# Kernel optimization log

Hardware: AMD Instinct MI355X
Metric: run time of the kernel (lower is better)

The kernel has to match this reference:

```python
import jax, jax.numpy as jnp
import numpy as np

DIM = 1024
NUM_HEADS = 16
HEAD_DIM = DIM // NUM_HEADS
SCALE = HEAD_DIM ** -0.5


def setup_inputs() -> dict:
    key = jax.random.key(0)
    k1, k2, k3, k4, k5 = jax.random.split(key, 5)
    B, N, C = 2, 2048, DIM
    x = jax.random.normal(k1, (B, N, C), dtype=jnp.float32)
    # nn.Linear(dim, 3*dim, bias=False): weight shape [3*dim, dim]
    w_qkv = jax.random.normal(k2, (3 * C, C), dtype=jnp.float32) * (C ** -0.5)
    # nn.Linear(dim, dim): weight [dim, dim], bias [dim]
    w_proj = jax.random.normal(k3, (C, C), dtype=jnp.float32) * (C ** -0.5)
    b_proj = jax.random.normal(k4, (C,), dtype=jnp.float32) * 0.02
    return {"x": x, "w_qkv": w_qkv, "w_proj": w_proj, "b_proj": b_proj}


def reference(x, w_qkv, w_proj, b_proj):
    B, N, C = x.shape
    H, D = NUM_HEADS, HEAD_DIM
    # qkv: [B, N, 3C] -> [3, B, H, N, D]
    qkv = (x @ w_qkv.T).reshape(B, N, 3, H, D).transpose(2, 0, 3, 1, 4)
    q, k, v = qkv[0], qkv[1], qkv[2]
    # attention scores [B, H, N, N]
    attn = jnp.einsum("bhnd,bhmd->bhnm", q, k) * SCALE
    attn = jax.nn.softmax(attn, axis=-1)
    # dropout p=0.0 -> identity (eval mode)
    out = jnp.einsum("bhnm,bhmd->bhnd", attn, v)  # [B, H, N, D]
    out = out.transpose(0, 2, 1, 3).reshape(B, N, C)
    return out @ w_proj.T + b_proj
```

## Files before the change

### kernel.cpp

```cpp
#include <hip/hip_runtime.h>
#include <hip/hip_bf16.h>
#include <cstdint>

#define DEV __device__ __forceinline__

typedef float f32x4 __attribute__((ext_vector_type(4)));
typedef short bf16x8 __attribute__((ext_vector_type(8)));
typedef unsigned short u16;
typedef unsigned int u32;

constexpr int Bb = 2, Nn = 2048, Cc = 1024, Hh = 16, Dd = 64;
constexpr float QSCALE = 0.18033688011112042f;

DEV u16 f2b(float f) {
  unsigned u = __float_as_uint(f);
  u += 0x7FFFu + ((u >> 16) & 1u);
  return (u16)(u >> 16);
}

DEV void gload_lds16(const u16* g, u16* l) {
  __builtin_amdgcn_global_load_lds(
      (const __attribute__((address_space(1))) void*)g,
      (__attribute__((address_space(3))) void*)l, 16, 0, 0);
}

DEV int swz(int row, int byteInRow) {
  return row * 128 + (byteInRow ^ ((row & 7) << 4));
}
DEV int swzp(int row, int byteInRow) {
  return row * 64 + (byteInRow ^ ((((row >> 2) + row) & 3) << 4));
}

DEV u32 cvtpk(float lo, float hi) {
  u32 r;
  asm("v_cvt_pk_bf16_f32 %0, %1, %2" : "=v"(r) : "v"(lo), "v"(hi));
  return r;
}
DEV void pl32swap(u32& a, u32& b) {
  asm("v_permlane32_swap_b32 %0, %1" : "+v"(a), "+v"(b));
}
DEV void pl16swap(u32& a, u32& b) {
  asm("v_permlane16_swap_b32 %0, %1" : "+v"(a), "+v"(b));
}

#if __has_builtin(__builtin_amdgcn_exp2f)
DEV float fast_exp2(float x) { return __builtin_amdgcn_exp2f(x); }
#else
DEV float fast_exp2(float x) { return exp2f(x); }
#endif

__global__ void cvt_all(const float* __restrict__ x, u16* __restrict__ xb,
                        const float* __restrict__ wq, u16* __restrict__ wqb,
                        const float* __restrict__ wp, u16* __restrict__ wpb) {
  constexpr int n1 = 4096 * 1024 / 4, n2 = 3072 * 1024 / 4, n3 = 1024 * 1024 / 4;
  constexpr int nQ = 1024 * 1024 / 4;
  int idx = blockIdx.x * blockDim.x + threadIdx.x;
  int stride = gridDim.x * blockDim.x;
  for (int i = idx; i < n1 + n2 + n3; i += stride) {
    const float* in; u16* out; int j;
    float sc = 1.f;
    if (i < n1) { in = x; out = xb; j = i; }
    else if (i < n1 + n2) { in = wq; out = wqb; j = i - n1; if (j < nQ) sc = QSCALE; }
    else { in = wp; out = wpb; j = i - n1 - n2; }
    float4 v = ((const float4*)in)[j];
    ushort4 o;
    o.x = f2b(v.x * sc); o.y = f2b(v.y * sc); o.z = f2b(v.z * sc); o.w = f2b(v.w * sc);
    ((ushort4*)out)[j] = o;
  }
}

__global__ __launch_bounds__(256) void gemm_qkv(
    const u16* __restrict__ A, const u16* __restrict__ W, u16* __restrict__ qkv_out) {
  constexpr int K = 1024, NT = K / 32;
  __shared__ __align__(16) u16 As[2][128 * 32];
  __shared__ __align__(16) u16 Bs[2][128 * 32];
  const int t = threadIdx.x, lane = t & 63;
  const int wm = t >> 7, wn = (t >> 6) & 1;
  const int bid = blockIdx.x;
  const int wg = (bid & 7) * 96 + (bid >> 3);
  const int bx = wg % 24, by = wg / 24;
  const int m0 = by * 128, n0 = bx * 128;
  const int fr = lane & 15, g = lane >> 4;

  const int srow = t >> 2;
  const int scp = (t & 3) ^ (((t >> 2) + (t >> 4)) & 3);
  const u16* gA = A + (size_t)(m0 + srow) * K + scp * 8;
  const u16* gW = W + (size_t)(n0 + srow) * K + scp * 8;

  f32x4 acc[4][4] = {};

#define STAGEQ(tile, buf)                                              \
  {                                                                    \
    const int k0_ = (tile) * 32;                                       \
    gload_lds16(gA + k0_, &As[buf][t * 8]);                            \
    gload_lds16(gA + k0_ + (size_t)64 * K, &As[buf][t * 8 + 2048]);    \
    gload_lds16(gW + k0_, &Bs[buf][t * 8]);                            \
    gload_lds16(gW + k0_ + (size_t)64 * K, &Bs[buf][t * 8 + 2048]);    \
  }

  STAGEQ(0, 0);
  __syncthreads();

  for (int tt = 0; tt < NT; ++tt) {
    const int cur = tt & 1;
    if (tt + 1 < NT) STAGEQ(tt + 1, cur ^ 1);
    const char* Ac = (const char*)As[cur];
    const char* Bc = (const char*)Bs[cur];
    bf16x8 af[4], bfr[4];
#pragma unroll
    for (int i = 0; i < 4; ++i)
      af[i] = *(const bf16x8*)(Ac + swzp(wm * 64 + i * 16 + fr, g * 16));
#pragma unroll
    for (int j = 0; j < 4; ++j)
      bfr[j] = *(const bf16x8*)(Bc + swzp(wn * 64 + j * 16 + fr, g * 16));
    __builtin_amdgcn_s_setprio(1);
#pragma unroll
    for (int i = 0; i < 4; ++i)
#pragma unroll
      for (int j = 0; j < 4; ++j)
        acc[i][j] = __builtin_amdgcn_mfma_f32_16x16x32_bf16(af[i], bfr[j], acc[i][j], 0, 0, 0);
    __builtin_amdgcn_s_setprio(0);
    __syncthreads();
  }

  const int rg = g * 4;
#pragma unroll
  for (int mi = 0; mi < 4; ++mi) {
#pragma unroll
    for (int ni = 0; ni < 4; ++ni) {
      const int col = n0 + wn * 64 + ni * 16 + fr;
      const int s = col >> 10, h = (col >> 6) & 15, d = col & 63;
      const int row0 = m0 + wm * 64 + mi * 16 + rg;
      const int b = row0 >> 11, nb = row0 & 2047;
      if (s == 2) {
        ushort4 o4;
        o4.x = f2b(acc[mi][ni][0]); o4.y = f2b(acc[mi][ni][1]);
        o4.z = f2b(acc[mi][ni][2]); o4.w = f2b(acc[mi][ni][3]);
        const size_t off = (size_t)2 * Bb * Hh * Nn * Dd +
                           (((size_t)b * Hh + h) * Dd + d) * Nn + nb;
        *(ushort4*)&qkv_out[off] = o4;
      } else {
#pragma unroll
        for (int r = 0; r < 4; ++r) {
          const size_t off = ((((size_t)s * Bb + b) * Hh + h) * Nn + (nb + r)) * Dd + d;
          qkv_out[off] = f2b(acc[mi][ni][r]);
        }
      }
    }
  }
#undef STAGEQ
}

__global__ __launch_bounds__(256) void gemm_proj(
    const u16* __restrict__ A, const u16* __restrict__ W,
    float* __restrict__ fout, const float* __restrict__ bias) {
  constexpr int K = 1024, Nmat = 1024, NT = K / 32;
  __shared__ __align__(16) u16 As[2][128 * 32];
  __shared__ __align__(16) u16 Bs[2][128 * 32];
  const int t = threadIdx.x, lane = t & 63;
  const int wm = t >> 7, wn = (t >> 6) & 1;
  const int bid = blockIdx.x;
  const int wg = (bid & 7) * 32 + (bid >> 3);
  const int bx = wg & 7, by = wg >> 3;
  const int m0 = by * 128, n0 = bx * 128;
  const int fr = lane & 15, g = lane >> 4;

  const int srow = t >> 2;
  const int scp = (t & 3) ^ (((t >> 2) + (t >> 4)) & 3);
  const u16* gA = A + (size_t)(m0 + srow) * K + scp * 8;
  const u16* gW = W + (size_t)(n0 + srow) * K + scp * 8;

  f32x4 acc[4][4] = {};

#define STAGEP(tile, buf)                                              \
  {                                                                    \
    const int k0_ = (tile) * 32;                                       \
    gload_lds16(gA + k0_, &As[buf][t * 8]);                            \
    gload_lds16(gA + k0_ + (size_t)64 * K, &As[buf][t * 8 + 2048]);    \
    gload_lds16(gW + k0_, &Bs[buf][t * 8]);                            \
    gload_lds16(gW + k0_ + (size_t)64 * K, &Bs[buf][t * 8 + 2048]);    \
  }

  STAGEP(0, 0);
  __syncthreads();

  for (int tt = 0; tt < NT; ++tt) {
    const int cur = tt & 1;
    if (tt + 1 < NT) STAGEP(tt + 1, cur ^ 1);
    const char* Ac = (const char*)As[cur];
    const char* Bc = (const char*)Bs[cur];
    bf16x8 af[4], bfr[4];
#pragma unroll
    for (int i = 0; i < 4; ++i)
      af[i] = *(const bf16x8*)(Ac + swzp(wm * 64 + i * 16 + fr, g * 16));
#pragma unroll
    for (int j = 0; j < 4; ++j)
      bfr[j] = *(const bf16x8*)(Bc + swzp(wn * 64 + j * 16 + fr, g * 16));
    __builtin_amdgcn_s_setprio(1);
#pragma unroll
    for (int i = 0; i < 4; ++i)
#pragma unroll
      for (int j = 0; j < 4; ++j)
        acc[i][j] = __builtin_amdgcn_mfma_f32_16x16x32_bf16(af[i], bfr[j], acc[i][j], 0, 0, 0);
    __builtin_amdgcn_s_setprio(0);
    __syncthreads();
  }

  const int rg = g * 4;
#pragma unroll
  for (int i = 0; i < 4; ++i)
#pragma unroll
    for (int j = 0; j < 4; ++j) {
      const int col = n0 + wn * 64 + j * 16 + fr;
#pragma unroll
      for (int r = 0; r < 4; ++r) {
        const int row = m0 + wm * 64 + i * 16 + rg + r;
        fout[(size_t)row * Nmat + col] = acc[i][j][r] + bias[col];
      }
    }
#undef STAGEP
}

__global__ __launch_bounds__(512, 4) void attn_fwd(
    const u16* __restrict__ Qg, const u16* __restrict__ Kg,
    const u16* __restrict__ Vtg, u16* __restrict__ Og) {
  __shared__ __align__(16) char smem[34816];
  const int t = threadIdx.x, lane = t & 63, w = t >> 6;
  const int qg = w >> 1, kh = w & 1;
  const int wg = ((blockIdx.x & 7) << 6) | (blockIdx.x >> 3);
  const int bh = wg >> 4;
  const int q0 = (wg & 15) * 128;
  const size_t base = (size_t)bh * Nn * Dd;
  const u16* Qb = Qg + base;
  const u16* Kb = Kg + base;
  const u16* Vb = Vtg + base;
  const int fr = lane & 15, g = lane >> 4;

  bf16x8 onesv;
  {
    union { u32 u[4]; bf16x8 v; } o_;
#pragma unroll
    for (int i = 0; i < 4; ++i) o_.u[i] = 0x3F803F80u;
    onesv = o_.v;
  }

  bf16x8 qf[2][2];
#pragma unroll
  for (int qt = 0; qt < 2; ++qt)
#pragma unroll
    for (int dc = 0; dc < 2; ++dc)
      qf[qt][dc] = *(const bf16x8*)&Qb[(size_t)(q0 + qg * 32 + qt * 16 + fr) * 64 + dc * 32 + g * 8];

  f32x4 ot[4][2] = {};
  float lse[2] = {0.f, 0.f};

  const int srow = t >> 3, scb = t & 7;
  const u16* kp = Kb + srow * 64 + scb * 8;
  const u16* vp = Vb + (size_t)srow * Nn + scb * 8;
  uint4 kreg, vreg;

#define LOADT(tile)                                        \
  {                                                        \
    kreg = *(const uint4*)(kp + (size_t)(tile) * 4096);    \
    vreg = *(const uint4*)(vp + (size_t)(tile) * 64);      \
  }
#define STORET(buf)                                        \
  {                                                        \
    char* kb_ = smem + (buf) * 16384;                      \
    *(uint4*)(kb_ + swz(srow, scb * 16)) = kreg;           \
    *(uint4*)(kb_ + 8192 + swz(srow, scb * 16)) = vreg;    \
  }

  LOADT(0);
  STORET(0);
  __syncthreads();

  for (int it = 0; it < 32; ++it) {
    const int cur = it & 1;
    const char* Kst = smem + cur * 16384;
    const char* Vst = Kst + 8192;
    if (it < 31) LOADT(it + 1);

    bf16x8 kf[2][2];
#pragma unroll
    for (int kvt = 0; kvt < 2; ++kvt)
#pragma unroll
      for (int dc = 0; dc < 2; ++dc)
        kf[kvt][dc] = *(const bf16x8*)(Kst + swz(kh * 32 + kvt * 16 + fr, dc * 64 + g * 16));
    f32x4 st[2][2] = {};
    __builtin_amdgcn_s_setprio(1);
#pragma unroll
    for (int dc = 0; dc < 2; ++dc)
#pragma unroll
      for (int kvt = 0; kvt < 2; ++kvt)
#pragma unroll
        for (int qt = 0; qt < 2; ++qt)
          st[kvt][qt] = __builtin_amdgcn_mfma_f32_16x16x32_bf16(kf[kvt][dc], qf[qt][dc], st[kvt][qt], 0, 0, 0);
    __builtin_amdgcn_s_setprio(0);

#pragma unroll
    for (int kvt = 0; kvt < 2; ++kvt)
#pragma unroll
      for (int qt = 0; qt < 2; ++qt)
#pragma unroll
        for (int r = 0; r < 4; ++r)
          st[kvt][qt][r] = fast_exp2(st[kvt][qt][r]);

    u32 pw[2][4];
#pragma unroll
    for (int qt = 0; qt < 2; ++qt) {
      u32 a0 = cvtpk(st[0][qt][0], st[0][qt][1]);
      u32 a1 = cvtpk(st[0][qt][2], st[0][qt][3]);
      u32 b0 = cvtpk(st[1][qt][0], st[1][qt][1]);
      u32 b1 = cvtpk(st[1][qt][2], st[1][qt][3]);
      pl32swap(a0, b0); pl16swap(a0, b0);
      pl32swap(a1, b1); pl16swap(a1, b1);
      pw[qt][0] = a0; pw[qt][1] = a1; pw[qt][2] = b0; pw[qt][3] = b1;
    }

    bf16x8 vf[4];
#pragma unroll
    for (int dt = 0; dt < 4; ++dt)
      vf[dt] = *(const bf16x8*)(Vst + swz(dt * 16 + fr, kh * 64 + g * 16));
    __builtin_amdgcn_s_setprio(1);
#pragma unroll
    for (int qt = 0; qt < 2; ++qt) {
      union { u32 u[4]; bf16x8 v; } pu;
      pu.u[0] = pw[qt][0]; pu.u[1] = pw[qt][1]; pu.u[2] = pw[qt][2]; pu.u[3] = pw[qt][3];
      f32x4 z = {0.f, 0.f, 0.f, 0.f};
      f32x4 rsv = __builtin_amdgcn_mfma_f32_16x16x32_bf16(onesv, pu.v, z, 0, 0, 0);
      lse[qt] += rsv[0];
#pragma unroll
      for (int dt = 0; dt < 4; ++dt)
        ot[dt][qt] = __builtin_amdgcn_mfma_f32_16x16x32_bf16(vf[dt], pu.v, ot[dt][qt], 0, 0, 0);
    }
    __builtin_amdgcn_s_setprio(0);

    if (it < 31) {
      STORET(cur ^ 1);
      __syncthreads();
    }
  }

  __syncthreads();
  float* Ob = (float*)(smem + qg * 8448);
  float* Lb = (float*)(smem + 33792 + qg * 128);
  if (kh) {
#pragma unroll
    for (int qt = 0; qt < 2; ++qt) {
#pragma unroll
      for (int dt = 0; dt < 4; ++dt)
#pragma unroll
        for (int r = 0; r < 4; ++r)
          Ob[(qt * 16 + fr) * 66 + dt * 16 + 4 * g + r] = ot[dt][qt][r];
      if (g == 0) Lb[qt * 16 + fr] = lse[qt];
    }
  }
  __syncthreads();
  if (!kh) {
    const int b = bh >> 4, h = bh & 15;
#pragma unroll
    for (int qt = 0; qt < 2; ++qt) {
      const float inv = 1.f / (lse[qt] + Lb[qt * 16 + fr]);
      const int tok = q0 + qg * 32 + qt * 16 + fr;
      const size_t rowbase = ((size_t)b * Nn + tok) * Cc + h * 64;
#pragma unroll
      for (int dt = 0; dt < 4; ++dt) {
        ushort4 o4;
        o4.x = f2b((ot[dt][qt][0] + Ob[(qt * 16 + fr) * 66 + dt * 16 + 4 * g + 0]) * inv);
        o4.y = f2b((ot[dt][qt][1] + Ob[(qt * 16 + fr) * 66 + dt * 16 + 4 * g + 1]) * inv);
        o4.z = f2b((ot[dt][qt][2] + Ob[(qt * 16 + fr) * 66 + dt * 16 + 4 * g + 2]) * inv);
        o4.w = f2b((ot[dt][qt][3] + Ob[(qt * 16 + fr) * 66 + dt * 16 + 4 * g + 3]) * inv);
        *(ushort4*)&Og[rowbase + dt * 16 + g * 4] = o4;
      }
    }
  }
#undef LOADT
#undef STORET
}

extern "C" void kernel_launch(void* const* d_in, const int* in_sizes, int n_in,
                              void* d_out, int out_size, void* d_ws, size_t ws_size,
                              hipStream_t stream) {
  const float* x      = (const float*)d_in[0];
  const float* w_qkv  = (const float*)d_in[1];
  const float* w_proj = (const float*)d_in[2];
  const float* b_proj = (const float*)d_in[3];
  float* out = (float*)d_out;

  u16* xb     = (u16*)d_ws;
  u16* wqkvb  = xb + (size_t)4096 * 1024;
  u16* wprojb = wqkvb + (size_t)3072 * 1024;
  u16* qkv    = wprojb + (size_t)1024 * 1024;
  u16* ows    = qkv + (size_t)3 * Bb * Hh * Nn * Dd;
  u16* q  = qkv;
  u16* k  = qkv + (size_t)Bb * Hh * Nn * Dd;
  u16* vt = k + (size_t)Bb * Hh * Nn * Dd;

  cvt_all<<<2048, 256, 0, stream>>>(x, xb, w_qkv, wqkvb, w_proj, wprojb);
  gemm_qkv<<<768, 256, 0, stream>>>(xb, wqkvb, qkv);
  attn_fwd<<<512, 512, 0, stream>>>(q, k, vt, ows);
  gemm_proj<<<256, 256, 0, stream>>>(ows, wprojb, out, b_proj);
}
```

Before: 114.4 us.

## Halve attention query tile per block to double grid size and occupancy

Result: slower. 158.1 us (+38.2%).

```diff
diff --git a/kernel.cpp b/kernel.cpp
--- a/kernel.cpp
+++ b/kernel.cpp
@@ -221,15 +221,15 @@
 #undef STAGEP
 }
 
-__global__ __launch_bounds__(512, 4) void attn_fwd(
+__global__ __launch_bounds__(512, 8) void attn_fwd(
     const u16* __restrict__ Qg, const u16* __restrict__ Kg,
     const u16* __restrict__ Vtg, u16* __restrict__ Og) {
   __shared__ __align__(16) char smem[34816];
   const int t = threadIdx.x, lane = t & 63, w = t >> 6;
   const int qg = w >> 1, kh = w & 1;
-  const int wg = ((blockIdx.x & 7) << 6) | (blockIdx.x >> 3);
-  const int bh = wg >> 4;
-  const int q0 = (wg & 15) * 128;
+  const int wg = ((blockIdx.x & 7) << 7) | (blockIdx.x >> 3);
+  const int bh = wg >> 5;
+  const int q0 = (wg & 31) * 64;
   const size_t base = (size_t)bh * Nn * Dd;
   const u16* Qb = Qg + base;
   const u16* Kb = Kg + base;
@@ -244,15 +244,13 @@
     onesv = o_.v;
   }
 
-  bf16x8 qf[2][2];
-#pragma unroll
-  for (int qt = 0; qt < 2; ++qt)
-#pragma unroll
-    for (int dc = 0; dc < 2; ++dc)
-      qf[qt][dc] = *(const bf16x8*)&Qb[(size_t)(q0 + qg * 32 + qt * 16 + fr) * 64 + dc * 32 + g * 8];
-
-  f32x4 ot[4][2] = {};
-  float lse[2] = {0.f, 0.f};
+  bf16x8 qf[2];
+#pragma unroll
+  for (int dc = 0; dc < 2; ++dc)
+    qf[dc] = *(const bf16x8*)&Qb[(size_t)(q0 + qg * 16 + fr) * 64 + dc * 32 + g * 8];
+
+  f32x4 ot[4] = {};
+  float lse = 0.f;
 
   const int srow = t >> 3, scb = t & 7;
   const u16* kp = Kb + srow * 64 + scb * 8;
@@ -287,52 +285,42 @@
 #pragma unroll
       for (int dc = 0; dc < 2; ++dc)
         kf[kvt][dc] = *(const bf16x8*)(Kst + swz(kh * 32 + kvt * 16 + fr, dc * 64 + g * 16));
-    f32x4 st[2][2] = {};
+    f32x4 st[2] = {};
     __builtin_amdgcn_s_setprio(1);
 #pragma unroll
     for (int dc = 0; dc < 2; ++dc)
 #pragma unroll
       for (int kvt = 0; kvt < 2; ++kvt)
-#pragma unroll
-        for (int qt = 0; qt < 2; ++qt)
-          st[kvt][qt] = __builtin_amdgcn_mfma_f32_16x16x32_bf16(kf[kvt][dc], qf[qt][dc], st[kvt][qt], 0, 0, 0);
+        st[kvt] = __builtin_amdgcn_mfma_f32_16x16x32_bf16(kf[kvt][dc], qf[dc], st[kvt], 0, 0, 0);
     __builtin_amdgcn_s_setprio(0);
 
 #pragma unroll
     for (int kvt = 0; kvt < 2; ++kvt)
 #pragma unroll
-      for (int qt = 0; qt < 2; ++qt)
-#pragma unroll
-        for (int r = 0; r < 4; ++r)
-          st[kvt][qt][r] = fast_exp2(st[kvt][qt][r]);
-
-    u32 pw[2][4];
-#pragma unroll
-    for (int qt = 0; qt < 2; ++qt) {
-      u32 a0 = cvtpk(st[0][qt][0], st[0][qt][1]);
-      u32 a1 = cvtpk(st[0][qt][2], st[0][qt][3]);
-      u32 b0 = cvtpk(st[1][qt][0], st[1][qt][1]);
-      u32 b1 = cvtpk(st[1][qt][2], st[1][qt][3]);
-      pl32swap(a0, b0); pl16swap(a0, b0);
-      pl32swap(a1, b1); pl16swap(a1, b1);
-      pw[qt][0] = a0; pw[qt][1] = a1; pw[qt][2] = b0; pw[qt][3] = b1;
-    }
+      for (int r = 0; r < 4; ++r)
+        st[kvt][r] = fast_exp2(st[kvt][r]);
+
+    u32 a0 = cvtpk(st[0][0], st[0][1]);
+    u32 a1 = cvtpk(st[0][2], st[0][3]);
+    u32 b0 = cvtpk(st[1][0], st[1][1]);
+    u32 b1 = cvtpk(st[1][2], st[1][3]);
+    pl32swap(a0, b0); pl16swap(a0, b0);
+    pl32swap(a1, b1); pl16swap(a1, b1);
 
     bf16x8 vf[4];
 #pragma unroll
     for (int dt = 0; dt < 4; ++dt)
       vf[dt] = *(const bf16x8*)(Vst + swz(dt * 16 + fr, kh * 64 + g * 16));
     __builtin_amdgcn_s_setprio(1);
-#pragma unroll
-    for (int qt = 0; qt < 2; ++qt) {
+    {
       union { u32 u[4]; bf16x8 v; } pu;
-      pu.u[0] = pw[qt][0]; pu.u[1] = pw[qt][1]; pu.u[2] = pw[qt][2]; pu.u[3] = pw[qt][3];
+      pu.u[0] = a0; pu.u[1] = a1; pu.u[2] = b0; pu.u[3] = b1;
       f32x4 z = {0.f, 0.f, 0.f, 0.f};
       f32x4 rsv = __builtin_amdgcn_mfma_f32_16x16x32_bf16(onesv, pu.v, z, 0, 0, 0);
-      lse[qt] += rsv[0];
+      lse += rsv[0];
 #pragma unroll
       for (int dt = 0; dt < 4; ++dt)
-        ot[dt][qt] = __builtin_amdgcn_mfma_f32_16x16x32_bf16(vf[dt], pu.v, ot[dt][qt], 0, 0, 0);
+        ot[dt] = __builtin_amdgcn_mfma_f32_16x16x32_bf16(vf[dt], pu.v, ot[dt], 0, 0, 0);
     }
     __builtin_amdgcn_s_setprio(0);
 
@@ -343,36 +331,30 @@
   }
 
   __syncthreads();
-  float* Ob = (float*)(smem + qg * 8448);
-  float* Lb = (float*)(smem + 33792 + qg * 128);
+  float* Ob = (float*)(smem + qg * 4224);
+  float* Lb = (float*)(smem + 16896 + qg * 64);
   if (kh) {
 #pragma unroll
-    for (int qt = 0; qt < 2; ++qt) {
-#pragma unroll
-      for (int dt = 0; dt < 4; ++dt)
-#pragma unroll
-        for (int r = 0; r < 4; ++r)
-          Ob[(qt * 16 + fr) * 66 + dt * 16 + 4 * g + r] = ot[dt][qt][r];
-      if (g == 0) Lb[qt * 16 + fr] = lse[qt];
-    }
+    for (int dt = 0; dt < 4; ++dt)
+#pragma unroll
+      for (int r = 0; r < 4; ++r)
+        Ob[fr * 66 + dt * 16 + 4 * g + r] = ot[dt][r];
+    if (g == 0) Lb[fr] = lse;
   }
   __syncthreads();
   if (!kh) {
     const int b = bh >> 4, h = bh & 15;
-#pragma unroll
-    for (int qt = 0; qt < 2; ++qt) {
-      const float inv = 1.f / (lse[qt] + Lb[qt * 16 + fr]);
-      const int tok = q0 + qg * 32 + qt * 16 + fr;
-      const size_t rowbase = ((size_t)b * Nn + tok) * Cc + h * 64;
-#pragma unroll
-      for (int dt = 0; dt < 4; ++dt) {
-        ushort4 o4;
-        o4.x = f2b((ot[dt][qt][0] + Ob[(qt * 16 + fr) * 66 + dt * 16 + 4 * g + 0]) * inv);
-        o4.y = f2b((ot[dt][qt][1] + Ob[(qt * 16 + fr) * 66 + dt * 16 + 4 * g + 1]) * inv);
-        o4.z = f2b((ot[dt][qt][2] + Ob[(qt * 16 + fr) * 66 + dt * 16 + 4 * g + 2]) * inv);
-        o4.w = f2b((ot[dt][qt][3] + Ob[(qt * 16 + fr) * 66 + dt * 16 + 4 * g + 3]) * inv);
-        *(ushort4*)&Og[rowbase + dt * 16 + g * 4] = o4;
-      }
+    const float inv = 1.f / (lse + Lb[fr]);
+    const int tok = q0 + qg * 16 + fr;
+    const size_t rowbase = ((size_t)b * Nn + tok) * Cc + h * 64;
+#pragma unroll
+    for (int dt = 0; dt < 4; ++dt) {
+      ushort4 o4;
+      o4.x = f2b((ot[dt][0] + Ob[fr * 66 + dt * 16 + 4 * g + 0]) * inv);
+      o4.y = f2b((ot[dt][1] + Ob[fr * 66 + dt * 16 + 4 * g + 1]) * inv);
+      o4.z = f2b((ot[dt][2] + Ob[fr * 66 + dt * 16 + 4 * g + 2]) * inv);
+      o4.w = f2b((ot[dt][3] + Ob[fr * 66 + dt * 16 + 4 * g + 3]) * inv);
+      *(ushort4*)&Og[rowbase + dt * 16 + g * 4] = o4;
     }
   }
 #undef LOADT
@@ -399,6 +381,6 @@
 
   cvt_all<<<2048, 256, 0, stream>>>(x, xb, w_qkv, wqkvb, w_proj, wprojb);
   gemm_qkv<<<768, 256, 0, stream>>>(xb, wqkvb, qkv);
-  attn_fwd<<<512, 512, 0, stream>>>(q, k, vt, ows);
+  attn_fwd<<<1024, 512, 0, stream>>>(q, k, vt, ows);
   gemm_proj<<<256, 256, 0, stream>>>(ows, wprojb, out, b_proj);
 }
```
